# Kernel tuning notes

Hardware: AMD Instinct MI355X
Metric: run time of the kernel (lower is better)

The kernel has to match this reference:

```python
import jax, jax.numpy as jnp
import numpy as np

B, L, V, E, H2, M, OOV = 128, 400, 50000, 512, 1024, 1024, 50


def setup_inputs() -> dict:
    key = jax.random.key(0)
    ks = jax.random.split(key, 14)
    s = 0.02
    return {
        "y": jax.random.randint(ks[0], (B,), 0, V),
        "h": jax.random.normal(ks[1], (1, B, H2), jnp.float32),
        "memory_bank": jax.random.normal(ks[2], (B, L, M), jnp.float32),
        "src_mask": jnp.ones((B, L), jnp.float32),
        "max_num_oovs": OOV,
        "src_oov": jax.random.randint(ks[3], (B, L), 0, V + OOV),
        # learned parameters (PyTorch Linear y = x @ W + b with W stored [in, out])
        "emb": jax.random.normal(ks[4], (V, E), jnp.float32) * s,
        "W_ih": jax.random.normal(ks[5], (E, 3 * H2), jnp.float32) * s,   # GRU input weights (r|z|n)
        "W_hh": jax.random.normal(ks[6], (H2, 3 * H2), jnp.float32) * s,  # GRU hidden weights (r|z|n)
        "b_ih": jnp.zeros((3 * H2,), jnp.float32),
        "b_hh": jnp.zeros((3 * H2,), jnp.float32),
        "W_mem": jax.random.normal(ks[7], (M, H2), jnp.float32) * s,      # attention memory_project (no bias)
        "W_dec": jax.random.normal(ks[8], (H2, H2), jnp.float32) * s,     # attention decode_project
        "b_dec": jnp.zeros((H2,), jnp.float32),
        "v": jax.random.normal(ks[9], (H2,), jnp.float32) * s,            # attention score vector (no bias)
        "W_pgen": jax.random.normal(ks[10], (M + H2 + E, 1), jnp.float32) * s,
        "b_pgen": jnp.zeros((1,), jnp.float32),
        "W_v1": jax.random.normal(ks[11], (M + H2, H2), jnp.float32) * s,
        "b_v1": jnp.zeros((H2,), jnp.float32),
        "W_v2": jax.random.normal(ks[12], (H2, V), jnp.float32) * s,
        "b_v2": jnp.zeros((V,), jnp.float32),
    }


def reference(y, h, memory_bank, src_mask, max_num_oovs, src_oov,
              emb, W_ih, W_hh, b_ih, b_hh, W_mem, W_dec, b_dec, v,
              W_pgen, b_pgen, W_v1, b_v1, W_v2, b_v2):
    # --- embedding lookup (single decode step) ---
    y_emb = emb[y]                                    # [B, E]
    h0 = h[-1]                                        # [B, H2]

    # --- one-step GRU (PyTorch gate order r, z, n); dropout is identity (eval) ---
    gi = y_emb @ W_ih + b_ih                          # [B, 3*H2]
    gh = h0 @ W_hh + b_hh
    i_r, i_z, i_n = jnp.split(gi, 3, axis=-1)
    h_r, h_z, h_n = jnp.split(gh, 3, axis=-1)
    r = jax.nn.sigmoid(i_r + h_r)
    z = jax.nn.sigmoid(i_z + h_z)
    n = jnp.tanh(i_n + r * h_n)
    h_next = (1.0 - z) * n + z * h0                   # [B, H2]

    # --- concat (Bahdanau) attention with masked softmax ---
    enc_feat = jnp.einsum('blm,mh->blh', memory_bank, W_mem)   # [B, L, H2]
    dec_feat = h_next @ W_dec + b_dec                           # [B, H2]
    scores = jnp.tanh(enc_feat + dec_feat[:, None, :]) @ v     # [B, L]
    attn = jax.nn.softmax(scores, axis=1) * src_mask
    attn_dist = attn / attn.sum(axis=1, keepdims=True)         # renormalized masked softmax
    context = jnp.einsum('bl,blm->bm', attn_dist, memory_bank) # [B, M]

    # --- vocab distribution ---
    vd_in = jnp.concatenate([context, h_next], axis=1)          # [B, M+H2]
    logits = (vd_in @ W_v1 + b_v1) @ W_v2 + b_v2                # [B, V]
    vocab_dist = jax.nn.softmax(logits, axis=1)

    # --- generation gate ---
    pg_in = jnp.concatenate([context, h_next, y_emb], axis=1)   # [B, M+H2+E]
    p_gen = jax.nn.sigmoid(pg_in @ W_pgen + b_pgen)             # [B, 1]

    # --- copy mechanism: scatter attention mass into extended vocab ---
    vocab_dist_ = p_gen * vocab_dist
    attn_dist_ = (1.0 - p_gen) * attn_dist
    bsz = vocab_dist_.shape[0]
    if max_num_oovs > 0:
        vocab_dist_ = jnp.concatenate(
            [vocab_dist_, jnp.zeros((bsz, max_num_oovs), vocab_dist_.dtype)], axis=1)
    rows = jnp.arange(bsz)[:, None]
    final_dist = vocab_dist_.at[rows, src_oov].add(attn_dist_)  # [B, V+OOV]

    return final_dist, h_next[None], context, attn_dist, p_gen
```

## Files before the change

### kernel.cpp

```cpp
#include <hip/hip_runtime.h>

#define B_   128
#define L_   400
#define V_   50000
#define E_   512
#define H2_  1024
#define M_   1024
#define OOV_ 50
#define VE_  50050
#define BL_  51200

typedef __attribute__((ext_vector_type(8))) short short8;
typedef __attribute__((ext_vector_type(4))) float f32x4;

__device__ __forceinline__ unsigned short f2bf(float f){
  unsigned int u = __builtin_bit_cast(unsigned int, f);
  u = (u + 0x7FFFu + ((u >> 16) & 1u)) >> 16;
  return (unsigned short)u;
}
__device__ __forceinline__ float bf2f(unsigned short s){
  unsigned int u = ((unsigned int)s) << 16;
  return __builtin_bit_cast(float, u);
}

__device__ __forceinline__ void gl_lds16(const void* g, void* l){
  __builtin_amdgcn_global_load_lds(
      (const __attribute__((address_space(1))) unsigned int*)g,
      (__attribute__((address_space(3))) unsigned int*)l, 16, 0, 0);
}

__device__ __forceinline__ float wredsum(float v){
  #pragma unroll
  for (int o = 32; o > 0; o >>= 1) v += __shfl_xor(v, o);
  return v;
}
__device__ __forceinline__ float wredmax(float v){
  #pragma unroll
  for (int o = 32; o > 0; o >>= 1) v = fmaxf(v, __shfl_xor(v, o));
  return v;
}

__device__ __forceinline__ void mb_convert_unit(const float* __restrict__ mb,
                                                unsigned char* __restrict__ mbT, int u){
  int gr  = u >> 7;
  int m16 = u & 127;
  const float* src = mb + (size_t)gr * 1024 + m16 * 8;
  float4 f0 = *(const float4*)src;
  float4 f1 = *(const float4*)(src + 4);
  uint4 w;
  w.x = (unsigned)f2bf(f0.x) | ((unsigned)f2bf(f0.y) << 16);
  w.y = (unsigned)f2bf(f0.z) | ((unsigned)f2bf(f0.w) << 16);
  w.z = (unsigned)f2bf(f1.x) | ((unsigned)f2bf(f1.y) << 16);
  w.w = (unsigned)f2bf(f1.z) | ((unsigned)f2bf(f1.w) << 16);
  int panel = gr >> 7, r = gr & 127;
  int ks = m16 >> 3, c16 = m16 & 7;
  size_t dst = (size_t)panel * 262144 + (size_t)ks * 16384
             + (size_t)((r * 128 + c16 * 16) ^ ((r & 7) << 4));
  *(uint4*)(mbT + dst) = w;
}

__global__ void pre_kernel(const float* __restrict__ mb, unsigned char* __restrict__ mbT,
                           const float* __restrict__ Wm, unsigned char* __restrict__ WTt,
                           const int* __restrict__ y, const float* __restrict__ emb,
                           float* __restrict__ yemb, float* __restrict__ zeroA,
                           float* __restrict__ ctx)
{
  __shared__ float tile[32][33];
  int bid = blockIdx.x, t = threadIdx.x;
  if (bid < 6400){
    mb_convert_unit(mb, mbT, bid * 256 + t);
  } else if (bid < 7424){
    int b2 = bid - 6400;
    int n0 = (b2 & 31) * 32, k0 = (b2 >> 5) * 32;
    int tx = t & 31, ty = t >> 5;
    #pragma unroll
    for (int i = 0; i < 32; i += 8) tile[ty + i][tx] = Wm[(size_t)(k0 + ty + i) * H2_ + n0 + tx];
    __syncthreads();
    if (t < 128){
      int nn = t & 31, k16 = t >> 5;
      int col = n0 + nn, kb = k0 + k16 * 8;
      uint4 w;
      w.x = (unsigned)f2bf(tile[k16*8+0][nn]) | ((unsigned)f2bf(tile[k16*8+1][nn]) << 16);
      w.y = (unsigned)f2bf(tile[k16*8+2][nn]) | ((unsigned)f2bf(tile[k16*8+3][nn]) << 16);
      w.z = (unsigned)f2bf(tile[k16*8+4][nn]) | ((unsigned)f2bf(tile[k16*8+5][nn]) << 16);
      w.w = (unsigned)f2bf(tile[k16*8+6][nn]) | ((unsigned)f2bf(tile[k16*8+7][nn]) << 16);
      int cpn = col >> 7, r = col & 127;
      int ks = kb >> 6, c16 = (kb & 63) >> 3;
      size_t dst = (size_t)cpn * 262144 + (size_t)ks * 16384
                 + (size_t)((r * 128 + c16 * 16) ^ ((r & 7) << 4));
      *(uint4*)(WTt + dst) = w;
    }
  } else if (bid < 7488){
    int idx = (bid - 7424) * 256 + t;
    int b  = idx >> 7;
    int c4 = (idx & 127) << 2;
    float4 v = *(const float4*)(emb + (size_t)y[b] * E_ + c4);
    *(float4*)(yemb + (size_t)b * E_ + c4) = v;
  } else if (bid < 8434){
    int u = (bid - 7488) * 256 + t;
    float4 z = {0.f, 0.f, 0.f, 0.f};
    *(float4*)(zeroA + (size_t)u * 4) = z;
  } else {
    int u = (bid - 8434) * 256 + t;
    float4 z = {0.f, 0.f, 0.f, 0.f};
    *(float4*)(ctx + (size_t)u * 4) = z;
  }
}

__device__ __forceinline__ void gemm128_body(int bx, int by,
                               const float* __restrict__ A, int lda,
                               const float* __restrict__ W, int ldw,
                               const float* __restrict__ bias,
                               float* __restrict__ C, int ldc,
                               int N, int kChunk, int addBias)
{
  int tid = threadIdx.x;
  int wv = tid >> 6, lane = tid & 63, lr = lane & 15, lhi = lane >> 4;
  int colBase = bx * 128 + wv * 32;
  int colL[2];
  colL[0] = min(colBase + lr, N - 1);
  colL[1] = min(colBase + 16 + lr, N - 1);
  int k0 = by * kChunk;

  f32x4 zero = {0.f, 0.f, 0.f, 0.f};
  f32x4 acc[8][2];
  #pragma unroll
  for (int r = 0; r < 8; r++){ acc[r][0] = zero; acc[r][1] = zero; }

  int nks = kChunk >> 5;
  for (int ks = 0; ks < nks; ++ks){
    int k = k0 + ks * 32 + lhi * 8;
    short8 bf[2];
    #pragma unroll
    for (int cf = 0; cf < 2; cf++){
      #pragma unroll
      for (int j = 0; j < 8; j++)
        bf[cf][j] = (short)f2bf(W[(size_t)(k + j) * ldw + colL[cf]]);
    }
    #pragma unroll
    for (int rf = 0; rf < 8; rf++){
      const float* ap = A + (size_t)(rf * 16 + lr) * lda + k;
      float4 a0 = *(const float4*)ap;
      float4 a1 = *(const float4*)(ap + 4);
      short8 af;
      af[0]=(short)f2bf(a0.x); af[1]=(short)f2bf(a0.y); af[2]=(short)f2bf(a0.z); af[3]=(short)f2bf(a0.w);
      af[4]=(short)f2bf(a1.x); af[5]=(short)f2bf(a1.y); af[6]=(short)f2bf(a1.z); af[7]=(short)f2bf(a1.w);
      acc[rf][0] = __builtin_amdgcn_mfma_f32_16x16x32_bf16(af, bf[0], acc[rf][0], 0, 0, 0);
      acc[rf][1] = __builtin_amdgcn_mfma_f32_16x16x32_bf16(af, bf[1], acc[rf][1], 0, 0, 0);
    }
  }

  bool addB = addBias && (by == 0);
  #pragma unroll
  for (int cf = 0; cf < 2; cf++){
    int col = colBase + cf * 16 + lr;
    bool ok = col < N;
    float bv = addB ? bias[colL[cf]] : 0.f;
    #pragma unroll
    for (int rf = 0; rf < 8; rf++)
      #pragma unroll
      for (int i = 0; i < 4; i++){
        int row = rf * 16 + lhi * 4 + i;
        if (ok) atomicAdd(&C[(size_t)row * ldc + col], acc[rf][cf][i] + bv);
      }
  }
}

__launch_bounds__(256)
__global__ void gigh_kernel(const float* __restrict__ yemb, const float* __restrict__ hin,
                            const float* __restrict__ W_ih, const float* __restrict__ W_hh,
                            float* __restrict__ gi, float* __restrict__ gh,
                            const float* __restrict__ mb, unsigned char* __restrict__ mbT){
  int bid = blockIdx.x;
  if (bid < 48)
    gemm128_body(bid % 24, bid / 24, yemb, E_,  W_ih, 3 * H2_, nullptr, gi, 3 * H2_, 3 * H2_, 256, 0);
  else if (bid < 144){
    int b2 = bid - 48;
    gemm128_body(b2 % 24, b2 / 24, hin, H2_, W_hh, 3 * H2_, nullptr, gh, 3 * H2_, 3 * H2_, 256, 0);
  } else {
    mb_convert_unit(mb, mbT, (6400 + bid - 144) * 256 + threadIdx.x);
  }
}

__global__ void gru_gates_kernel(const float* __restrict__ gi, const float* __restrict__ gh,
                                 const float* __restrict__ bih, const float* __restrict__ bhh,
                                 const float* __restrict__ h0, float* __restrict__ hn,
                                 const float* __restrict__ mb, unsigned char* __restrict__ mbT){
  int bid = blockIdx.x;
  if (bid >= 512){
    mb_convert_unit(mb, mbT, (12800 + bid - 512) * 256 + threadIdx.x);
    return;
  }
  int idx = bid * 256 + threadIdx.x;
  int b = idx >> 10, j = idx & 1023;
  const float* gib = gi + (size_t)b * 3072;
  const float* ghb = gh + (size_t)b * 3072;
  float ir = gib[j]        + bih[j],        hr = ghb[j]        + bhh[j];
  float iz = gib[j + 1024] + bih[j + 1024], hz = ghb[j + 1024] + bhh[j + 1024];
  float in_= gib[j + 2048] + bih[j + 2048], hnv= ghb[j + 2048] + bhh[j + 2048];
  float r = 1.f / (1.f + __expf(-(ir + hr)));
  float z = 1.f / (1.f + __expf(-(iz + hz)));
  float n = tanhf(in_ + r * hnv);
  hn[idx] = (1.f - z) * n + z * h0[idx];
}

__launch_bounds__(256)
__global__ void dec_kernel(const float* __restrict__ hnext, const float* __restrict__ W_dec,
                           const float* __restrict__ b_dec, float* __restrict__ dec,
                           const float* __restrict__ mb, unsigned char* __restrict__ mbT){
  int bid = blockIdx.x;
  if (bid < 32)
    gemm128_body(bid & 7, bid >> 3, hnext, H2_, W_dec, H2_, b_dec, dec, H2_, H2_, 256, 1);
  else
    mb_convert_unit(mb, mbT, (19200 + bid - 32) * 256 + threadIdx.x);
}

__launch_bounds__(256)
__global__ void scores_kernel(const unsigned char* __restrict__ mbT,
                              const unsigned char* __restrict__ WTt,
                              const float* __restrict__ dec, const float* __restrict__ vvec,
                              float* __restrict__ scr)
{
  __shared__ __align__(16) unsigned char LDSm[65536];
  const int tid = threadIdx.x, lane = tid & 63;
  const int wv = tid >> 6, lr = lane & 15, lhi = lane >> 4;
  const int wru = wv >> 1, wcu = wv & 1;

  int p = blockIdx.x;
  int lid = (p & 7) * 400 + (p >> 3);
  int rp = lid >> 3, cp = lid & 7;
  int r0 = rp << 7;

  int wvu = __builtin_amdgcn_readfirstlane(wv);
  const unsigned char* segA = mbT + (size_t)rp * 262144 + wvu * 4096 + lane * 16;
  const unsigned char* segB = WTt + (size_t)cp * 262144 + wvu * 4096 + lane * 16;
  const int ldsA = wvu * 4096;
  const int ldsB = 16384 + wvu * 4096;

  int aoff[4], boff[4];
  #pragma unroll
  for (int rf = 0; rf < 4; rf++){
    int row = wru * 64 + rf * 16 + lr;
    aoff[rf] = (row * 128 + lhi * 16) ^ ((row & 7) << 4);
  }
  #pragma unroll
  for (int cf = 0; cf < 4; cf++){
    int col = wcu * 64 + cf * 16 + lr;
    boff[cf] = ((col * 128 + lhi * 16) ^ ((col & 7) << 4)) + 16384;
  }

  f32x4 zero = {0.f, 0.f, 0.f, 0.f};
  f32x4 acc[4][4];
  #pragma unroll
  for (int rf = 0; rf < 4; rf++)
    #pragma unroll
    for (int cf = 0; cf < 4; cf++) acc[rf][cf] = zero;

  #pragma unroll
  for (int j = 0; j < 4; j++){
    gl_lds16(segA + j * 1024, &LDSm[ldsA + j * 1024]);
    gl_lds16(segB + j * 1024, &LDSm[ldsB + j * 1024]);
  }

  #pragma unroll 1
  for (int t = 0; t < 16; ++t){
    const int cur = (t & 1) << 15;
    if (t < 15){
      const size_t soff = (size_t)(t + 1) * 16384;
      const int nb = ((t + 1) & 1) << 15;
      #pragma unroll
      for (int j = 0; j < 4; j++){
        gl_lds16(segA + soff + j * 1024, &LDSm[nb + ldsA + j * 1024]);
        gl_lds16(segB + soff + j * 1024, &LDSm[nb + ldsB + j * 1024]);
      }
      asm volatile("s_waitcnt vmcnt(8)" ::: "memory");
    } else {
      asm volatile("s_waitcnt vmcnt(0)" ::: "memory");
    }
    __builtin_amdgcn_sched_barrier(0);
    __builtin_amdgcn_s_barrier();
    __builtin_amdgcn_sched_barrier(0);
    #pragma unroll
    for (int k2 = 0; k2 < 2; k2++){
      short8 af[4], bfr[4];
      #pragma unroll
      for (int rf = 0; rf < 4; rf++) af[rf]  = *(const short8*)&LDSm[cur + (aoff[rf] ^ (k2 << 6))];
      #pragma unroll
      for (int cf = 0; cf < 4; cf++) bfr[cf] = *(const short8*)&LDSm[cur + (boff[cf] ^ (k2 << 6))];
      __builtin_amdgcn_s_setprio(1);
      #pragma unroll
      for (int rf = 0; rf < 4; rf++)
        #pragma unroll
        for (int cf = 0; cf < 4; cf++)
          acc[rf][cf] = __builtin_amdgcn_mfma_f32_16x16x32_bf16(af[rf], bfr[cf], acc[rf][cf], 0, 0, 0);
      __builtin_amdgcn_s_setprio(0);
    }
    __builtin_amdgcn_sched_barrier(0);
    asm volatile("s_waitcnt lgkmcnt(0)" ::: "memory");
    __builtin_amdgcn_s_barrier();
    __builtin_amdgcn_sched_barrier(0);
  }

  int colb = (cp << 7) + wcu * 64 + lr;
  float vv0 = vvec[colb], vv1 = vvec[colb + 16], vv2 = vvec[colb + 32], vv3 = vvec[colb + 48];
  #pragma unroll
  for (int rf = 0; rf < 4; rf++){
    #pragma unroll
    for (int i = 0; i < 4; i++){
      int grow = r0 + wru * 64 + rf * 16 + lhi * 4 + i;
      int bb = grow / 400;
      const float* dp = dec + (size_t)bb * 1024 + colb;
      float x0 = acc[rf][0][i] + dp[0];
      float x1 = acc[rf][1][i] + dp[16];
      float x2 = acc[rf][2][i] + dp[32];
      float x3 = acc[rf][3][i] + dp[48];
      float part = (1.f - 2.f / (__expf(2.f * x0) + 1.f)) * vv0
                 + (1.f - 2.f / (__expf(2.f * x1) + 1.f)) * vv1
                 + (1.f - 2.f / (__expf(2.f * x2) + 1.f)) * vv2
                 + (1.f - 2.f / (__expf(2.f * x3) + 1.f)) * vv3;
      part += __shfl_xor(part, 1);
      part += __shfl_xor(part, 2);
      part += __shfl_xor(part, 4);
      part += __shfl_xor(part, 8);
      if (lr == 0) atomicAdd(&scr[grow], part);
    }
  }
}

__launch_bounds__(256)
__global__ void context_kernel(const float* __restrict__ scr, const float* __restrict__ mask,
                               const unsigned char* __restrict__ mbT,
                               float* __restrict__ ctx, float* __restrict__ attn){
  int b = blockIdx.y, lc = blockIdx.x, t = threadIdx.x;
  int wv = t >> 6, lane = t & 63;
  __shared__ float red[4];
  __shared__ float a[400];
  float s0 = scr[b * 400 + t];
  float s1 = (t < 144) ? scr[b * 400 + t + 256] : -1e30f;
  float m = wredmax(fmaxf(s0, s1));
  if (lane == 0) red[wv] = m;
  __syncthreads();
  float M = fmaxf(fmaxf(red[0], red[1]), fmaxf(red[2], red[3]));
  __syncthreads();
  float e0 = __expf(s0 - M) * mask[b * 400 + t];
  float e1 = (t < 144) ? __expf(s1 - M) * mask[b * 400 + t + 256] : 0.f;
  float s = wredsum(e0 + e1);
  if (lane == 0) red[wv] = s;
  __syncthreads();
  float inv = 1.f / (red[0] + red[1] + red[2] + red[3]);
  a[t] = e0 * inv;
  if (t < 144) a[t + 256] = e1 * inv;
  __syncthreads();
  if (t < 100) attn[b * 400 + lc * 100 + t] = a[lc * 100 + t];

  int u = t & 127;
  int half = t >> 7;
  int ks = u >> 3, c16 = u & 7;
  float sa[8];
  #pragma unroll
  for (int j = 0; j < 8; j++) sa[j] = 0.f;
  for (int l = half; l < 100; l += 2){
    int gr = b * 400 + lc * 100 + l;
    int panel = gr >> 7, r = gr & 127;
    const unsigned char* pp = mbT + (size_t)panel * 262144 + (size_t)ks * 16384
                              + (size_t)((r * 128 + c16 * 16) ^ ((r & 7) << 4));
    short8 v = *(const short8*)pp;
    float al = a[lc * 100 + l];
    #pragma unroll
    for (int j = 0; j < 8; j++) sa[j] += al * bf2f((unsigned short)v[j]);
  }
  float* cp = ctx + (size_t)b * M_ + u * 8;
  #pragma unroll
  for (int j = 0; j < 8; j++) atomicAdd(cp + j, sa[j]);
}

__launch_bounds__(256)
__global__ void v1_pgen_kernel(const float* __restrict__ ctx, const float* __restrict__ hn,
                               const float* __restrict__ yemb,
                               const float* __restrict__ Wv1, const float* __restrict__ bv1,
                               float* __restrict__ vp,
                               const float* __restrict__ Wp, const float* __restrict__ bp,
                               float* __restrict__ pg)
{
  int bid = blockIdx.x;
  if (bid < 64){
    int bx = bid & 7, by = bid >> 3;
    int tid = threadIdx.x;
    int wv = tid >> 6, lane = tid & 63, lr = lane & 15, lhi = lane >> 4;
    int colBase = bx * 128 + wv * 32;
    const float* Asrc = (by < 4) ? ctx : hn;
    int k0 = ((by < 4) ? by : (by - 4)) * 256;
    int wk0 = by * 256;

    f32x4 zero = {0.f, 0.f, 0.f, 0.f};
    f32x4 acc[8][2];
    #pragma unroll
    for (int r = 0; r < 8; r++){ acc[r][0] = zero; acc[r][1] = zero; }

    for (int ks = 0; ks < 8; ++ks){
      int k  = k0 + ks * 32 + lhi * 8;
      int wk = wk0 + ks * 32 + lhi * 8;
      short8 bf[2];
      #pragma unroll
      for (int cf = 0; cf < 2; cf++){
        #pragma unroll
        for (int j = 0; j < 8; j++)
          bf[cf][j] = (short)f2bf(Wv1[(size_t)(wk + j) * H2_ + colBase + cf * 16 + lr]);
      }
      #pragma unroll
      for (int rf = 0; rf < 8; rf++){
        const float* ap = Asrc + (size_t)(rf * 16 + lr) * 1024 + k;
        float4 a0 = *(const float4*)ap;
        float4 a1 = *(const float4*)(ap + 4);
        short8 af;
        af[0]=(short)f2bf(a0.x); af[1]=(short)f2bf(a0.y); af[2]=(short)f2bf(a0.z); af[3]=(short)f2bf(a0.w);
        af[4]=(short)f2bf(a1.x); af[5]=(short)f2bf(a1.y); af[6]=(short)f2bf(a1.z); af[7]=(short)f2bf(a1.w);
        acc[rf][0] = __builtin_amdgcn_mfma_f32_16x16x32_bf16(af, bf[0], acc[rf][0], 0, 0, 0);
        acc[rf][1] = __builtin_amdgcn_mfma_f32_16x16x32_bf16(af, bf[1], acc[rf][1], 0, 0, 0);
      }
    }

    float* Cw = vp + (size_t)by * 131072;
    bool addB = (by == 0);
    #pragma unroll
    for (int cf = 0; cf < 2; cf++){
      int col = colBase + cf * 16 + lr;
      float bv = addB ? bv1[col] : 0.f;
      #pragma unroll
      for (int rf = 0; rf < 8; rf++)
        #pragma unroll
        for (int i = 0; i < 4; i++){
          int row = rf * 16 + lhi * 4 + i;
          Cw[(size_t)row * H2_ + col] = acc[rf][cf][i] + bv;
        }
    }
  } else {
    int b = bid - 64, t = threadIdx.x, wv = t >> 6, lane = t & 63;
    __shared__ float red[4];
    float s = 0.f;
    for (int i = t; i < 1024; i += 256) s += ctx[(size_t)b * 1024 + i] * Wp[i];
    for (int i = t; i < 1024; i += 256) s += hn[(size_t)b * 1024 + i] * Wp[1024 + i];
    for (int i = t; i < 512;  i += 256) s += yemb[(size_t)b * 512 + i] * Wp[2048 + i];
    s = wredsum(s);
    if (lane == 0) red[wv] = s;
    __syncthreads();
    if (t == 0){
      float S = red[0] + red[1] + red[2] + red[3] + bp[0];
      pg[b] = 1.f / (1.f + __expf(-S));
    }
  }
}

__global__ void hid2bf_kernel(const float* __restrict__ vp, unsigned short* __restrict__ hb){
  int id = blockIdx.x * 256 + threadIdx.x;
  float4 s = *(const float4*)(vp + (size_t)id * 4);
  #pragma unroll
  for (int ky = 1; ky < 8; ky++){
    float4 v = *(const float4*)(vp + (size_t)ky * 131072 + (size_t)id * 4);
    s.x += v.x; s.y += v.y; s.z += v.z; s.w += v.w;
  }
  ushort2 p0 = {f2bf(s.x), f2bf(s.y)};
  ushort2 p1 = {f2bf(s.z), f2bf(s.w)};
  *(ushort2*)(hb + (size_t)id * 4)     = p0;
  *(ushort2*)(hb + (size_t)id * 4 + 2) = p1;
}

__launch_bounds__(256)
__global__ void gemm_bfA_kernel(const unsigned short* __restrict__ A,
                                const float* __restrict__ W,
                                const float* __restrict__ bias,
                                float* __restrict__ C0, float* __restrict__ C1,
                                int N, int kChunk)
{
  int tid = threadIdx.x;
  int wv = tid >> 6, lane = tid & 63, lr = lane & 15, lhi = lane >> 4;
  int colBase = blockIdx.x * 128 + wv * 32;
  int colL[2];
  colL[0] = min(colBase + lr, N - 1);
  colL[1] = min(colBase + 16 + lr, N - 1);
  int k0 = blockIdx.y * kChunk;
  float* Cw = (blockIdx.y == 0) ? C0 : C1;

  f32x4 zero = {0.f, 0.f, 0.f, 0.f};
  f32x4 acc[8][2];
  #pragma unroll
  for (int r = 0; r < 8; r++){ acc[r][0] = zero; acc[r][1] = zero; }

  int nks = kChunk >> 5;
  for (int ks = 0; ks < nks; ++ks){
    int k = k0 + ks * 32 + lhi * 8;
    short8 bf[2];
    #pragma unroll
    for (int cf = 0; cf < 2; cf++){
      #pragma unroll
      for (int j = 0; j < 8; j++)
        bf[cf][j] = (short)f2bf(W[(size_t)(k + j) * N + colL[cf]]);
    }
    #pragma unroll
    for (int rf = 0; rf < 8; rf++){
      short8 af = *(const short8*)(A + (size_t)(rf * 16 + lr) * 1024 + k);
      acc[rf][0] = __builtin_amdgcn_mfma_f32_16x16x32_bf16(af, bf[0], acc[rf][0], 0, 0, 0);
      acc[rf][1] = __builtin_amdgcn_mfma_f32_16x16x32_bf16(af, bf[1], acc[rf][1], 0, 0, 0);
    }
  }

  bool addB = (blockIdx.y == 0);
  #pragma unroll
  for (int cf = 0; cf < 2; cf++){
    int col = colBase + cf * 16 + lr;
    bool ok = col < N;
    float bv = addB ? bias[colL[cf]] : 0.f;
    #pragma unroll
    for (int rf = 0; rf < 8; rf++)
      #pragma unroll
      for (int i = 0; i < 4; i++){
        int row = rf * 16 + lhi * 4 + i;
        if (ok) Cw[(size_t)row * V_ + col] = acc[rf][cf][i] + bv;
      }
  }
}

__global__ void vocab_softmax_kernel(float* __restrict__ lg0, const float* __restrict__ lg1,
                                     const float* __restrict__ pg,
                                     const float* __restrict__ attn, const int* __restrict__ soov,
                                     float* __restrict__ fin){
  int b = blockIdx.x, t = threadIdx.x, wv = t >> 6, lane = t & 63;
  __shared__ float redm[16], reds[16];
  float* l0 = lg0 + (size_t)b * V_;
  const float* l1 = lg1 + (size_t)b * V_;
  float m = -1e30f, s = 0.f;
  for (int i = t; i < V_; i += 1024){
    float l = l0[i] + l1[i];
    l0[i] = l;
    float mn = fmaxf(m, l);
    s = s * __expf(m - mn) + __expf(l - mn);
    m = mn;
  }
  #pragma unroll
  for (int o = 32; o > 0; o >>= 1){
    float mo = __shfl_xor(m, o), so = __shfl_xor(s, o);
    float mn = fmaxf(m, mo);
    s = s * __expf(m - mn) + so * __expf(mo - mn);
    m = mn;
  }
  if (lane == 0){ redm[wv] = m; reds[wv] = s; }
  __syncthreads();
  float M = -1e30f;
  #pragma unroll
  for (int w = 0; w < 16; w++) M = fmaxf(M, redm[w]);
  float S = 0.f;
  #pragma unroll
  for (int w = 0; w < 16; w++) S += reds[w] * __expf(redm[w] - M);
  float pgb = pg[b];
  float scale = pgb / S;
  float* fb = fin + (size_t)b * VE_;
  for (int i = t; i < V_; i += 1024) fb[i] = __expf(l0[i] - M) * scale;
  for (int i = V_ + t; i < VE_; i += 1024) fb[i] = 0.f;
  __syncthreads();
  float om = 1.f - pgb;
  if (t < 400) atomicAdd(&fb[soov[b * 400 + t]], om * attn[b * 400 + t]);
}

extern "C" void kernel_launch(void* const* d_in, const int* in_sizes, int n_in,
                              void* d_out, int out_size, void* d_ws, size_t ws_size,
                              hipStream_t stream)
{
  const int*   y     = (const int*)  d_in[0];
  const float* hin   = (const float*)d_in[1];
  const float* mb    = (const float*)d_in[2];
  const float* mask  = (const float*)d_in[3];
  const int*   soov  = (const int*)  d_in[5];
  const float* emb   = (const float*)d_in[6];
  const float* W_ih  = (const float*)d_in[7];
  const float* W_hh  = (const float*)d_in[8];
  const float* b_ih  = (const float*)d_in[9];
  const float* b_hh  = (const float*)d_in[10];
  const float* W_mem = (const float*)d_in[11];
  const float* W_dec = (const float*)d_in[12];
  const float* b_dec = (const float*)d_in[13];
  const float* vvec  = (const float*)d_in[14];
  const float* W_pg  = (const float*)d_in[15];
  const float* b_pg  = (const float*)d_in[16];
  const float* W_v1  = (const float*)d_in[17];
  const float* b_v1  = (const float*)d_in[18];
  const float* W_v2  = (const float*)d_in[19];
  const float* b_v2  = (const float*)d_in[20];

  float* out   = (float*)d_out;
  float* fin   = out;
  float* hnext = out + (size_t)B_ * VE_;
  float* ctx   = hnext + (size_t)B_ * H2_;
  float* attn  = ctx + (size_t)B_ * M_;
  float* pg    = attn + (size_t)B_ * L_;

  float* ws   = (float*)d_ws;
  float* yemb = ws;
  float* gi   = ws + 65536;
  float* gh   = gi + 393216;
  float* dec  = gh + 393216;
  float* scr  = dec + 131072;
  float* lg0  = scr + 51200;
  float* vp   = lg0;
  unsigned short* hidbf = (unsigned short*)(lg0 + 6400000);
  unsigned char*  WTt   = (unsigned char*)(hidbf + 131072);
  unsigned char*  mbT   = WTt + 2097152;
  float* lg1  = (float*)mbT;

  pre_kernel<<<8562, 256, 0, stream>>>(mb, mbT, W_mem, WTt, y, emb, yemb, gi, ctx);
  gigh_kernel<<<6544, 256, 0, stream>>>(yemb, hin, W_ih, W_hh, gi, gh, mb, mbT);
  gru_gates_kernel<<<6912, 256, 0, stream>>>(gi, gh, b_ih, b_hh, hin, hnext, mb, mbT);
  dec_kernel<<<6432, 256, 0, stream>>>(hnext, W_dec, b_dec, dec, mb, mbT);

  scores_kernel<<<3200, 256, 0, stream>>>(mbT, WTt, dec, vvec, scr);
  context_kernel<<<dim3(4, 128), 256, 0, stream>>>(scr, mask, mbT, ctx, attn);

  v1_pgen_kernel<<<192, 256, 0, stream>>>(ctx, hnext, yemb, W_v1, b_v1, vp, W_pg, b_pg, pg);
  hid2bf_kernel<<<128, 256, 0, stream>>>(vp, hidbf);
  gemm_bfA_kernel<<<dim3(391, 2), 256, 0, stream>>>(hidbf, W_v2, b_v2, lg0, lg1, V_, 512);

  vocab_softmax_kernel<<<128, 1024, 0, stream>>>(lg0, lg1, pg, attn, soov, fin);
}
```

Before: 521.2 us.

## Drop split-K in vocab GEMM and simplify scores-kernel pipeline sync

The vocab projection GEMM no longer splits K across two grid slices writing separate partial-logit buffers. Each block now covers the full K=1024, so the second logits buffer and the partial-sum add-and-writeback in the vocab softmax go away. Separately, the scores kernel loses its MFMA priority hints, the explicit LDS waitcnt before the trailing barrier, and one scheduling barrier, which loosens synchronisation in its main loop. The trade-off is half as many GEMM blocks to hide the latency of the strided fp32 weight loads, and that the scores kernel now relies on the compiler's own LDS waits.

```diff
diff --git a/kernel.cpp b/kernel.cpp
--- a/kernel.cpp
+++ b/kernel.cpp
@@ -277,9 +277,9 @@
     } else {
       asm volatile("s_waitcnt vmcnt(0)" ::: "memory");
     }
-    __builtin_amdgcn_sched_barrier(0);
     __builtin_amdgcn_s_barrier();
     __builtin_amdgcn_sched_barrier(0);
+
     #pragma unroll
     for (int k2 = 0; k2 < 2; k2++){
       short8 af[4], bfr[4];
@@ -287,16 +287,14 @@
       for (int rf = 0; rf < 4; rf++) af[rf]  = *(const short8*)&LDSm[cur + (aoff[rf] ^ (k2 << 6))];
       #pragma unroll
       for (int cf = 0; cf < 4; cf++) bfr[cf] = *(const short8*)&LDSm[cur + (boff[cf] ^ (k2 << 6))];
-      __builtin_amdgcn_s_setprio(1);
       #pragma unroll
       for (int rf = 0; rf < 4; rf++)
         #pragma unroll
         for (int cf = 0; cf < 4; cf++)
           acc[rf][cf] = __builtin_amdgcn_mfma_f32_16x16x32_bf16(af[rf], bfr[cf], acc[rf][cf], 0, 0, 0);
-      __builtin_amdgcn_s_setprio(0);
-    }
+    }
+
     __builtin_amdgcn_sched_barrier(0);
-    asm volatile("s_waitcnt lgkmcnt(0)" ::: "memory");
     __builtin_amdgcn_s_barrier();
     __builtin_amdgcn_sched_barrier(0);
   }
@@ -469,8 +467,7 @@
 __global__ void gemm_bfA_kernel(const unsigned short* __restrict__ A,
                                 const float* __restrict__ W,
                                 const float* __restrict__ bias,
-                                float* __restrict__ C0, float* __restrict__ C1,
-                                int N, int kChunk)
+                                float* __restrict__ C, int N)
 {
   int tid = threadIdx.x;
   int wv = tid >> 6, lane = tid & 63, lr = lane & 15, lhi = lane >> 4;
@@ -478,17 +475,14 @@
   int colL[2];
   colL[0] = min(colBase + lr, N - 1);
   colL[1] = min(colBase + 16 + lr, N - 1);
-  int k0 = blockIdx.y * kChunk;
-  float* Cw = (blockIdx.y == 0) ? C0 : C1;
 
   f32x4 zero = {0.f, 0.f, 0.f, 0.f};
   f32x4 acc[8][2];
   #pragma unroll
   for (int r = 0; r < 8; r++){ acc[r][0] = zero; acc[r][1] = zero; }
 
-  int nks = kChunk >> 5;
-  for (int ks = 0; ks < nks; ++ks){
-    int k = k0 + ks * 32 + lhi * 8;
+  for (int ks = 0; ks < 32; ++ks){
+    int k = ks * 32 + lhi * 8;
     short8 bf[2];
     #pragma unroll
     for (int cf = 0; cf < 2; cf++){
@@ -504,34 +498,30 @@
     }
   }
 
-  bool addB = (blockIdx.y == 0);
   #pragma unroll
   for (int cf = 0; cf < 2; cf++){
     int col = colBase + cf * 16 + lr;
     bool ok = col < N;
-    float bv = addB ? bias[colL[cf]] : 0.f;
+    float bv = bias[colL[cf]];
     #pragma unroll
     for (int rf = 0; rf < 8; rf++)
       #pragma unroll
       for (int i = 0; i < 4; i++){
         int row = rf * 16 + lhi * 4 + i;
-        if (ok) Cw[(size_t)row * V_ + col] = acc[rf][cf][i] + bv;
+        if (ok) C[(size_t)row * V_ + col] = acc[rf][cf][i] + bv;
       }
   }
 }
 
-__global__ void vocab_softmax_kernel(float* __restrict__ lg0, const float* __restrict__ lg1,
-                                     const float* __restrict__ pg,
+__global__ void vocab_softmax_kernel(const float* __restrict__ lg0, const float* __restrict__ pg,
                                      const float* __restrict__ attn, const int* __restrict__ soov,
                                      float* __restrict__ fin){
   int b = blockIdx.x, t = threadIdx.x, wv = t >> 6, lane = t & 63;
   __shared__ float redm[16], reds[16];
-  float* l0 = lg0 + (size_t)b * V_;
-  const float* l1 = lg1 + (size_t)b * V_;
+  const float* l0 = lg0 + (size_t)b * V_;
   float m = -1e30f, s = 0.f;
   for (int i = t; i < V_; i += 1024){
-    float l = l0[i] + l1[i];
-    l0[i] = l;
+    float l = l0[i];
     float mn = fmaxf(m, l);
     s = s * __expf(m - mn) + __expf(l - mn);
     m = mn;
@@ -604,7 +594,6 @@
   unsigned short* hidbf = (unsigned short*)(lg0 + 6400000);
   unsigned char*  WTt   = (unsigned char*)(hidbf + 131072);
   unsigned char*  mbT   = WTt + 2097152;
-  float* lg1  = (float*)mbT;
 
   pre_kernel<<<8562, 256, 0, stream>>>(mb, mbT, W_mem, WTt, y, emb, yemb, gi, ctx);
   gigh_kernel<<<6544, 256, 0, stream>>>(yemb, hin, W_ih, W_hh, gi, gh, mb, mbT);
@@ -616,7 +605,7 @@
 
   v1_pgen_kernel<<<192, 256, 0, stream>>>(ctx, hnext, yemb, W_v1, b_v1, vp, W_pg, b_pg, pg);
   hid2bf_kernel<<<128, 256, 0, stream>>>(vp, hidbf);
-  gemm_bfA_kernel<<<dim3(391, 2), 256, 0, stream>>>(hidbf, W_v2, b_v2, lg0, lg1, V_, 512);
-
-  vocab_softmax_kernel<<<128, 1024, 0, stream>>>(lg0, lg1, pg, attn, soov, fin);
-}
+  gemm_bfA_kernel<<<391, 256, 0, stream>>>(hidbf, W_v2, b_v2, lg0, V_);
+
+  vocab_softmax_kernel<<<128, 1024, 0, stream>>>(lg0, pg, attn, soov, fin);
+}
```

New measurement: 504.1 us. 3.3% less time.
